# Optimization experiments

Hardware: AMD Instinct MI355X
Metric: run time of the kernel (lower is better)

Reference implementation:

```python
import jax, jax.numpy as jnp
import numpy as np

D_MODEL = 1024
N_HEADS = 16
D_K = D_MODEL // N_HEADS
B, S = 2, 2048


def setup_inputs() -> dict:
    key = jax.random.key(0)
    ks = jax.random.split(key, 9)
    scale = 1.0 / np.sqrt(D_MODEL)
    x = jax.random.normal(ks[0], (B, S, D_MODEL), dtype=jnp.float32)
    # causal mask, broadcastable to [B, H, S, S]; mask==0 -> masked
    mask = jnp.tril(jnp.ones((S, S), dtype=bool))[None, None]
    wq = jax.random.normal(ks[1], (D_MODEL, D_MODEL), dtype=jnp.float32) * scale
    bq = jnp.zeros((D_MODEL,), dtype=jnp.float32)
    wk = jax.random.normal(ks[2], (D_MODEL, D_K), dtype=jnp.float32) * scale
    bk = jnp.zeros((D_K,), dtype=jnp.float32)
    wv = jax.random.normal(ks[3], (D_MODEL, D_K), dtype=jnp.float32) * scale
    bv = jnp.zeros((D_K,), dtype=jnp.float32)
    wo = jax.random.normal(ks[4], (D_MODEL, D_MODEL), dtype=jnp.float32) * scale
    bo = jnp.zeros((D_MODEL,), dtype=jnp.float32)
    return {"x": x, "mask": mask, "wq": wq, "bq": bq, "wk": wk, "bk": bk,
            "wv": wv, "bv": bv, "wo": wo, "bo": bo}


def reference(x, mask, wq, bq, wk, bk, wv, bv, wo, bo):
    b, s, d = x.shape
    h, dk = N_HEADS, D_K
    q = (x @ wq + bq).reshape(b, s, h, dk)            # [b,s,h,dk]
    k = x @ wk + bk                                    # [b,s,dk] shared across heads (MQA)
    v = x @ wv + bv                                    # [b,s,dk]
    scores = jnp.einsum('bshd,btd->bhst', q, k) / jnp.sqrt(jnp.float32(dk))
    scores = jnp.where(mask, scores, jnp.float32(-1e9))
    attn = jax.nn.softmax(scores, axis=-1)             # [b,h,s,t]
    out = jnp.einsum('bhst,btd->bshd', attn, v).reshape(b, s, d)
    return out @ wo + bo
```

## Files before the change

### kernel.cpp

```cpp
#include <hip/hip_runtime.h>
#include <hip/hip_bf16.h>
#include <stdint.h>


typedef __attribute__((ext_vector_type(8))) short short8;
typedef __attribute__((ext_vector_type(4))) short short4_t;
typedef __attribute__((ext_vector_type(4))) float f32x4;

#define MFMA16(a, b, c) __builtin_amdgcn_mfma_f32_16x16x32_bf16((a), (b), (c), 0, 0, 0)

#define SCALE_Q 0.1803368801111244f

__device__ inline void gload_lds16(const void* g, void* l) {
  __builtin_amdgcn_global_load_lds(
      (const __attribute__((address_space(1))) void*)g,
      (__attribute__((address_space(3))) void*)l, 16, 0, 0);
}

__device__ inline float fast_exp2(float x) {
  float r;
  asm("v_exp_f32 %0, %1" : "=v"(r) : "v"(x));
  return r;
}

__device__ inline short f2bf(float f) {
  union { float f; uint32_t u; } v;
  v.f = f;
  uint32_t u = v.u;
  return (short)((u + 0x7fffu + ((u >> 16) & 1u)) >> 16);
}

__device__ inline uint32_t pk_bf16(float lo, float hi) {
  uint32_t r;
  asm("v_cvt_pk_bf16_f32 %0, %1, %2" : "=v"(r) : "v"(lo), "v"(hi));
  return r;
}

__device__ inline int imin(int a, int b) { return a < b ? a : b; }

__global__ __launch_bounds__(256) void k_prep(
    const float* __restrict__ x, const float* __restrict__ wq,
    const float* __restrict__ wk, const float* __restrict__ wv,
    const float* __restrict__ bq, const float* __restrict__ bk,
    const float* __restrict__ bv, const float* __restrict__ wo,
    short* __restrict__ xb, short* __restrict__ wqkvt,
    float* __restrict__ biasq, short* __restrict__ wot) {
  const int blk = blockIdx.x;
  const int t = threadIdx.x;
  if (blk >= 545) {
    const int base = (blk - 545) * 8192;
#pragma unroll
    for (int it = 0; it < 4; ++it) {
      const int i = base + it * 2048 + t * 8;
      const float* xp = x + i;
      short8 o;
#pragma unroll
      for (int j = 0; j < 8; ++j) o[j] = f2bf(xp[j]);
      *(short8*)(xb + i) = o;
    }
    return;
  }
  if (blk == 544) {
    for (int idx = t; idx < 1152; idx += 256)
      biasq[idx] = idx < 1024 ? bq[idx] * SCALE_Q
                              : (idx < 1088 ? bk[idx - 1024] : bv[idx - 1088]);
    return;
  }
  __shared__ float lds[64][65];
  const int j = blk;
  const float* src;
  short* dst;
  int ncol, k0, n0, row0;
  float sc = 1.f;
  if (j < 256)      { src = wq; dst = wqkvt; ncol = 1024; k0 = (j >> 4) * 64;
                      n0 = (j & 15) * 64; row0 = n0; sc = SCALE_Q; }
  else if (j < 272) { src = wk; dst = wqkvt; ncol = 64; k0 = (j - 256) * 64;
                      n0 = 0; row0 = 1024; }
  else if (j < 288) { src = wv; dst = wqkvt; ncol = 64; k0 = (j - 272) * 64;
                      n0 = 0; row0 = 1088; }
  else              { int jj = j - 288; src = wo; dst = wot; ncol = 1024;
                      k0 = (jj >> 4) * 64; n0 = (jj & 15) * 64; row0 = n0; }
#pragma unroll
  for (int i = 0; i < 4; ++i) {
    int f = i * 256 + t;
    int k = f >> 4, c = f & 15;
    const float* sp = src + (size_t)(k0 + k) * ncol + n0 + c * 4;
#pragma unroll
    for (int q = 0; q < 4; ++q) lds[k][c * 4 + q] = sp[q];
  }
  __syncthreads();
#pragma unroll
  for (int i = 0; i < 2; ++i) {
    int f = i * 256 + t;
    int n = f >> 3, kc = f & 7;
    short8 o;
#pragma unroll
    for (int q = 0; q < 8; ++q) o[q] = f2bf(lds[kc * 8 + q][n] * sc);
    *(short8*)(dst + (size_t)(row0 + n) * 1024 + k0 + kc * 8) = o;
  }
}

__global__ __launch_bounds__(256, 3) void k_gemm(const short* __restrict__ A,
                                                 const short* __restrict__ Bt,
                                                 const float* __restrict__ bias,
                                                 void* __restrict__ C, int ldc,
                                                 int out_bf16,
                                                 short* __restrict__ vt_out) {
  __shared__ short As[2][4096];
  __shared__ short Bs[2][8192];
  const int t = threadIdx.x;
  const int w = t >> 6, l = t & 63;
  const int l15 = l & 15, lhi = l >> 4;
  const int m0 = blockIdx.x * 64, n0 = blockIdx.y * 128;

  f32x4 acc[4][2];
#pragma unroll
  for (int i = 0; i < 4; ++i)
#pragma unroll
    for (int j = 0; j < 2; ++j)
#pragma unroll
      for (int r = 0; r < 4; ++r) acc[i][j][r] = 0.f;

  const int fA0 = w * 64 + l;
  const int rA0 = fA0 >> 3, gA0 = (fA0 & 7) ^ (rA0 & 7);
  const int fA1 = fA0 + 256;
  const int rA1 = fA1 >> 3, gA1 = (fA1 & 7) ^ (rA1 & 7);

  const int aoff = l15 * 128 + ((lhi ^ (l15 & 7)) << 4);
  const int coff = l15 * 128 + (((4 + lhi) ^ (l15 & 7)) << 4);

#define GEMM_STAGE(buf, k0)                                                    \
  {                                                                            \
    gload_lds16(A + (size_t)(m0 + rA0) * 1024 + (k0) + gA0 * 8,               \
                &As[buf][w * 512]);                                            \
    gload_lds16(A + (size_t)(m0 + rA1) * 1024 + (k0) + gA1 * 8,               \
                &As[buf][2048 + w * 512]);                                     \
    _Pragma("unroll")                                                          \
    for (int q = 0; q < 4; ++q) {                                              \
      int f = q * 256 + fA0;                                                   \
      int r = f >> 3, gc = (f & 7) ^ (r & 7);                                  \
      gload_lds16(Bt + (size_t)(n0 + r) * 1024 + (k0) + gc * 8,               \
                  &Bs[buf][q * 2048 + w * 512]);                               \
    }                                                                          \
  }

  GEMM_STAGE(0, 0);

  for (int ks = 0; ks < 16; ++ks) {
    const int nb = (ks + 1) & 1;
    GEMM_STAGE(nb, imin(ks + 1, 15) * 64);
    asm volatile("s_waitcnt vmcnt(6)" ::: "memory");

    const char* as = (const char*)&As[ks & 1][0];
    const char* bs = (const char*)&Bs[ks & 1][0];
    short8 afA[4], afB[4], bfA[2], bfB[2];
#pragma unroll
    for (int i = 0; i < 4; ++i) {
      afA[i] = *(const short8*)(as + i * 2048 + aoff);
      afB[i] = *(const short8*)(as + i * 2048 + coff);
    }
#pragma unroll
    for (int j = 0; j < 2; ++j) {
      bfA[j] = *(const short8*)(bs + (w * 32 + j * 16) * 128 + aoff);
      bfB[j] = *(const short8*)(bs + (w * 32 + j * 16) * 128 + coff);
    }
#pragma unroll
    for (int i = 0; i < 4; ++i)
#pragma unroll
      for (int j = 0; j < 2; ++j) {
        acc[i][j] = MFMA16(afA[i], bfA[j], acc[i][j]);
        acc[i][j] = MFMA16(afB[i], bfB[j], acc[i][j]);
      }
    __builtin_amdgcn_s_barrier();
  }
  asm volatile("s_waitcnt vmcnt(0)" ::: "memory");

#pragma unroll
  for (int j = 0; j < 2; ++j) {
    int col = n0 + w * 32 + j * 16 + l15;
    float bia = bias[col];
#pragma unroll
    for (int i = 0; i < 4; ++i) {
      int row0 = m0 + i * 16 + lhi * 4;
      if (out_bf16) {
#pragma unroll
        for (int r = 0; r < 4; ++r)
          ((short*)C)[(size_t)(row0 + r) * ldc + col] =
              (short)(pk_bf16(acc[i][j][r] + bia, 0.f) & 0xffff);
        if (vt_out != nullptr && col >= 1088) {
          const int d = col - 1088;
          const int bb = row0 >> 11, rho = row0 & 2047;
          const int T = rho >> 6, y = rho & 63;
          const int pb = 16 * ((y >> 3) & 1) + 8 * ((y >> 2) & 1) +
                         4 * ((y >> 5) & 1) + 2 * ((y >> 4) & 1);
          short* vp = vt_out + (size_t)(bb * 64 + d) * 2048 + T * 64 + pb;
          *(uint32_t*)(vp) = pk_bf16(acc[i][j][0] + bia, acc[i][j][1] + bia);
          *(uint32_t*)(vp + 32) = pk_bf16(acc[i][j][2] + bia, acc[i][j][3] + bia);
        }
      } else {
#pragma unroll
        for (int r = 0; r < 4; ++r)
          ((float*)C)[(size_t)(row0 + r) * ldc + col] = acc[i][j][r] + bia;
      }
    }
  }
#undef GEMM_STAGE
}

__global__ __launch_bounds__(512, 4) void k_attn(const short* __restrict__ qkv,
                                                 const short* __restrict__ vt,
                                                 short* __restrict__ attnb) {
  __shared__ char smem[65536];
  const int t = threadIdx.x;
  const int w = t >> 6, l = t & 63;
  const int l15 = l & 15, lhi = l >> 4;
  const int qw = w & 3, g2 = w >> 2;
  const int bx = blockIdx.x;
  const int o = bx >> 5, gg = o & 7;
  const int p = (o < 8) ? gg : 15 - gg;
  const int bh = bx & 31, b = bh >> 4, h = bh & 15;
  const int nph = p + 1;
  const short* kb = qkv + (size_t)(b * 2048) * 1152 + 1024;
  const short* vb = vt + (size_t)b * 64 * 2048;

  const int srow = w * 8 + (l >> 3);
  const int gcol = (l & 7) ^ (l >> 3);
  const short* kS = kb + (size_t)srow * 1152 + gcol * 8;
  const short* vS = vb + (size_t)srow * 2048 + gcol * 8;

  const int aoff = l15 * 128 + ((lhi ^ (l15 & 7)) << 4);
  const int coff = l15 * 128 + (((4 + lhi) ^ (l15 & 7)) << 4);

  short8 ones;
#pragma unroll
  for (int j = 0; j < 8; ++j) ones[j] = (short)0x3F80;

  const int qbase = p * 128 + qw * 32;
  const int myq0 = qbase + l15;
  const int myq1 = qbase + 16 + l15;
  const int ttdiag = qbase >> 6;

  const short* qp0 = qkv + (size_t)(b * 2048 + myq0) * 1152 + h * 64 + 8 * lhi;
  const short* qp1 = qkv + (size_t)(b * 2048 + myq1) * 1152 + h * 64 + 8 * lhi;
  short8 qa0 = *(const short8*)(qp0);
  short8 qc0 = *(const short8*)(qp0 + 32);
  short8 qa1 = *(const short8*)(qp1);
  short8 qc1 = *(const short8*)(qp1 + 32);

  f32x4 oo[2][4], o5a, o5b;
#pragma unroll
  for (int qg = 0; qg < 2; ++qg)
#pragma unroll
    for (int fd = 0; fd < 4; ++fd)
#pragma unroll
      for (int r = 0; r < 4; ++r) oo[qg][fd][r] = 0.f;
#pragma unroll
  for (int r = 0; r < 4; ++r) { o5a[r] = 0.f; o5b[r] = 0.f; }

  gload_lds16(kS, smem + w * 1024);
  gload_lds16(kS + 73728, smem + 16384 + w * 1024);
  gload_lds16(vS, smem + 32768 + w * 1024);
  gload_lds16(vS + 64, smem + 32768 + 16384 + w * 1024);
  __syncthreads();

#pragma unroll 1
  for (int i = 0; i < nph; ++i) {
    if (i + 1 < nph) {
      const int nb = (i + 1) & 1;
      const size_t ko2 = (size_t)(2 * i + 2) * 73728;
      const int vo2 = (2 * i + 2) * 64;
      gload_lds16(kS + ko2, smem + nb * 8192 + w * 1024);
      gload_lds16(kS + ko2 + 73728, smem + 16384 + nb * 8192 + w * 1024);
      gload_lds16(vS + vo2, smem + 32768 + nb * 8192 + w * 1024);
      gload_lds16(vS + vo2 + 64, smem + 32768 + 16384 + nb * 8192 + w * 1024);
      __builtin_amdgcn_sched_barrier(0);
    }

    const int tt = 2 * i + g2;
    const int cb = i & 1;

    const char* kr = smem + g2 * 16384 + cb * 8192;
    f32x4 s0[4], s1[4];
    __builtin_amdgcn_s_setprio(1);
#pragma unroll
    for (int f = 0; f < 4; ++f) {
      short8 ka = *(const short8*)(kr + f * 2048 + aoff);
      short8 kc = *(const short8*)(kr + f * 2048 + coff);
      f32x4 z0 = {0.f, 0.f, 0.f, 0.f};
      z0 = MFMA16(ka, qa0, z0);
      z0 = MFMA16(kc, qc0, z0);
      s0[f] = z0;
      f32x4 z1 = {0.f, 0.f, 0.f, 0.f};
      z1 = MFMA16(ka, qa1, z1);
      z1 = MFMA16(kc, qc1, z1);
      s1[f] = z1;
    }
    __builtin_amdgcn_s_setprio(0);

    if (tt >= ttdiag) {
      const int t0 = tt * 64;
#pragma unroll
      for (int f = 0; f < 4; ++f) {
        int kvb = t0 + f * 16 + lhi * 4;
#pragma unroll
        for (int r = 0; r < 4; ++r) {
          s0[f][r] = (kvb + r <= myq0) ? s0[f][r] : -1e30f;
          s1[f][r] = (kvb + r <= myq1) ? s1[f][r] : -1e30f;
        }
      }
    }

#pragma unroll
    for (int f = 0; f < 4; ++f)
#pragma unroll
      for (int r = 0; r < 4; ++r) {
        s0[f][r] = fast_exp2(s0[f][r]);
        s1[f][r] = fast_exp2(s1[f][r]);
      }

    union { short8 v; uint32_t d[4]; } pA0, pB0, pA1, pB1;
#pragma unroll
    for (int f = 0; f < 4; ++f) {
      pA0.d[f] = pk_bf16(s0[f][0], s0[f][1]);
      pB0.d[f] = pk_bf16(s0[f][2], s0[f][3]);
      pA1.d[f] = pk_bf16(s1[f][0], s1[f][1]);
      pB1.d[f] = pk_bf16(s1[f][2], s1[f][3]);
    }

    const char* vr = smem + 32768 + g2 * 16384 + cb * 8192;
    __builtin_amdgcn_s_setprio(1);
#pragma unroll
    for (int fd = 0; fd < 4; ++fd) {
      short8 va = *(const short8*)(vr + fd * 2048 + aoff);
      short8 vc = *(const short8*)(vr + fd * 2048 + coff);
      oo[0][fd] = MFMA16(va, pA0.v, oo[0][fd]);
      oo[0][fd] = MFMA16(vc, pB0.v, oo[0][fd]);
      oo[1][fd] = MFMA16(va, pA1.v, oo[1][fd]);
      oo[1][fd] = MFMA16(vc, pB1.v, oo[1][fd]);
    }
    o5a = MFMA16(ones, pA0.v, o5a);
    o5a = MFMA16(ones, pB0.v, o5a);
    o5b = MFMA16(ones, pA1.v, o5b);
    o5b = MFMA16(ones, pB1.v, o5b);
    __builtin_amdgcn_s_setprio(0);

    __syncthreads();
  }

  float* scr = (float*)smem;
  float* sp = scr + ((qw << 6) + l) * 34;
  if (g2 == 1) {
#pragma unroll
    for (int qg = 0; qg < 2; ++qg)
#pragma unroll
      for (int fd = 0; fd < 4; ++fd)
#pragma unroll
        for (int r = 0; r < 4; ++r) sp[qg * 16 + fd * 4 + r] = oo[qg][fd][r];
    sp[32] = o5a[0];
    sp[33] = o5b[0];
  }
  __syncthreads();
  if (g2 == 0) {
#pragma unroll
    for (int qg = 0; qg < 2; ++qg) {
      float lsum = (qg ? o5b[0] : o5a[0]) + sp[32 + qg];
      float inv = 1.f / lsum;
      int myq = qbase + qg * 16 + l15;
      short* op = attnb + (size_t)(b * 2048 + myq) * 1024 + h * 64;
#pragma unroll
      for (int fd = 0; fd < 4; ++fd) {
        union { short4_t s4; uint32_t d[2]; } ov;
        float v0 = (oo[qg][fd][0] + sp[qg * 16 + fd * 4 + 0]) * inv;
        float v1 = (oo[qg][fd][1] + sp[qg * 16 + fd * 4 + 1]) * inv;
        float v2 = (oo[qg][fd][2] + sp[qg * 16 + fd * 4 + 2]) * inv;
        float v3 = (oo[qg][fd][3] + sp[qg * 16 + fd * 4 + 3]) * inv;
        ov.d[0] = pk_bf16(v0, v1);
        ov.d[1] = pk_bf16(v2, v3);
        *(short4_t*)(op + fd * 16 + lhi * 4) = ov.s4;
      }
    }
  }
}

extern "C" void kernel_launch(void* const* d_in, const int* in_sizes, int n_in,
                              void* d_out, int out_size, void* d_ws, size_t ws_size,
                              hipStream_t stream) {
  const float* x  = (const float*)d_in[0];
  const float* wq = (const float*)d_in[2];
  const float* bq = (const float*)d_in[3];
  const float* wk = (const float*)d_in[4];
  const float* bk = (const float*)d_in[5];
  const float* wv = (const float*)d_in[6];
  const float* bv = (const float*)d_in[7];
  const float* wo = (const float*)d_in[8];
  const float* bo = (const float*)d_in[9];

  char* ws = (char*)d_ws;
  short* xb    = (short*)(ws + 0);
  short* qkv   = (short*)(ws + 8388608);
  short* wqkvt = (short*)(ws + 17825792);
  short* wot   = (short*)(ws + 20185088);
  short* vt    = (short*)(ws + 22282240);
  short* attnb = (short*)(ws + 22806528);
  float* biasq = (float*)(ws + 31195136);

  k_prep<<<1057, 256, 0, stream>>>(x, wq, wk, wv, bq, bk, bv, wo,
                                   xb, wqkvt, biasq, wot);
  k_gemm<<<dim3(64, 9), 256, 0, stream>>>(xb, wqkvt, biasq, qkv, 1152, 1, vt);
  k_attn<<<512, 512, 0, stream>>>(qkv, vt, attnb);
  k_gemm<<<dim3(64, 8), 256, 0, stream>>>(attnb, wot, bo, d_out, 1024, 0,
                                          nullptr);
}
```

Baseline: 69.66 us.

## Split attention KV range across four wave groups with 1024-thread blocks

```diff
diff --git a/kernel.cpp b/kernel.cpp
--- a/kernel.cpp
+++ b/kernel.cpp
@@ -207,26 +207,29 @@
 #undef GEMM_STAGE
 }
 
-__global__ __launch_bounds__(512, 4) void k_attn(const short* __restrict__ qkv,
-                                                 const short* __restrict__ vt,
-                                                 short* __restrict__ attnb) {
+__global__ __launch_bounds__(1024, 4) void k_attn(const short* __restrict__ qkv,
+                                                  const short* __restrict__ vt,
+                                                  short* __restrict__ attnb) {
   __shared__ char smem[65536];
   const int t = threadIdx.x;
   const int w = t >> 6, l = t & 63;
   const int l15 = l & 15, lhi = l >> 4;
-  const int qw = w & 3, g2 = w >> 2;
+  const int qw = w >> 2, kvg = w & 3;
   const int bx = blockIdx.x;
-  const int o = bx >> 5, gg = o & 7;
-  const int p = (o < 8) ? gg : 15 - gg;
+  const int o = bx >> 5;
+  const int p = 15 - o;
   const int bh = bx & 31, b = bh >> 4, h = bh & 15;
-  const int nph = p + 1;
+  const int nph = (2 * p + 5) >> 2;
   const short* kb = qkv + (size_t)(b * 2048) * 1152 + 1024;
   const short* vb = vt + (size_t)b * 64 * 2048;
 
-  const int srow = w * 8 + (l >> 3);
-  const int gcol = (l & 7) ^ (l >> 3);
-  const short* kS = kb + (size_t)srow * 1152 + gcol * 8;
-  const short* vS = vb + (size_t)srow * 2048 + gcol * 8;
+  const int f0 = t, f1 = t + 1024;
+  const int kR0 = (f0 >> 3) & 63, kJ0 = f0 >> 9, kG0 = (f0 & 7) ^ (kR0 & 7);
+  const int kR1 = (f1 >> 3) & 63, kJ1 = f1 >> 9, kG1 = (f1 & 7) ^ (kR1 & 7);
+  const short* kS0 = kb + (size_t)(kJ0 * 64 + kR0) * 1152 + kG0 * 8;
+  const short* kS1 = kb + (size_t)(kJ1 * 64 + kR1) * 1152 + kG1 * 8;
+  const short* vS0 = vb + (size_t)kR0 * 2048 + kJ0 * 64 + kG0 * 8;
+  const short* vS1 = vb + (size_t)kR1 * 2048 + kJ1 * 64 + kG1 * 8;
 
   const int aoff = l15 * 128 + ((lhi ^ (l15 & 7)) << 4);
   const int coff = l15 * 128 + (((4 + lhi) ^ (l15 & 7)) << 4);
@@ -257,29 +260,20 @@
 #pragma unroll
   for (int r = 0; r < 4; ++r) { o5a[r] = 0.f; o5b[r] = 0.f; }
 
-  gload_lds16(kS, smem + w * 1024);
-  gload_lds16(kS + 73728, smem + 16384 + w * 1024);
-  gload_lds16(vS, smem + 32768 + w * 1024);
-  gload_lds16(vS + 64, smem + 32768 + 16384 + w * 1024);
-  __syncthreads();
-
 #pragma unroll 1
   for (int i = 0; i < nph; ++i) {
-    if (i + 1 < nph) {
-      const int nb = (i + 1) & 1;
-      const size_t ko2 = (size_t)(2 * i + 2) * 73728;
-      const int vo2 = (2 * i + 2) * 64;
-      gload_lds16(kS + ko2, smem + nb * 8192 + w * 1024);
-      gload_lds16(kS + ko2 + 73728, smem + 16384 + nb * 8192 + w * 1024);
-      gload_lds16(vS + vo2, smem + 32768 + nb * 8192 + w * 1024);
-      gload_lds16(vS + vo2 + 64, smem + 32768 + 16384 + nb * 8192 + w * 1024);
-      __builtin_amdgcn_sched_barrier(0);
-    }
-
-    const int tt = 2 * i + g2;
-    const int cb = i & 1;
-
-    const char* kr = smem + g2 * 16384 + cb * 8192;
+    const size_t ko = (size_t)(4 * i) * 73728;
+    const int vo = 4 * i * 64;
+    gload_lds16(kS0 + ko, smem + f0 * 16);
+    gload_lds16(kS1 + ko, smem + f1 * 16);
+    gload_lds16(vS0 + vo, smem + 32768 + f0 * 16);
+    gload_lds16(vS1 + vo, smem + 32768 + f1 * 16);
+    asm volatile("s_waitcnt vmcnt(0)" ::: "memory");
+    __builtin_amdgcn_s_barrier();
+
+    const int tt = 4 * i + kvg;
+
+    const char* kr = (const char*)smem + kvg * 8192;
     f32x4 s0[4], s1[4];
     __builtin_amdgcn_s_setprio(1);
 #pragma unroll
@@ -298,10 +292,10 @@
     __builtin_amdgcn_s_setprio(0);
 
     if (tt >= ttdiag) {
-      const int t0 = tt * 64;
+      const int t0m = tt * 64;
 #pragma unroll
       for (int f = 0; f < 4; ++f) {
-        int kvb = t0 + f * 16 + lhi * 4;
+        int kvb = t0m + f * 16 + lhi * 4;
 #pragma unroll
         for (int r = 0; r < 4; ++r) {
           s0[f][r] = (kvb + r <= myq0) ? s0[f][r] : -1e30f;
@@ -327,7 +321,7 @@
       pB1.d[f] = pk_bf16(s1[f][2], s1[f][3]);
     }
 
-    const char* vr = smem + 32768 + g2 * 16384 + cb * 8192;
+    const char* vr = (const char*)smem + 32768 + kvg * 8192;
     __builtin_amdgcn_s_setprio(1);
 #pragma unroll
     for (int fd = 0; fd < 4; ++fd) {
@@ -344,42 +338,64 @@
     o5b = MFMA16(ones, pB1.v, o5b);
     __builtin_amdgcn_s_setprio(0);
 
-    __syncthreads();
+    __builtin_amdgcn_s_barrier();
   }
 
   float* scr = (float*)smem;
-  float* sp = scr + ((qw << 6) + l) * 34;
-  if (g2 == 1) {
-#pragma unroll
-    for (int qg = 0; qg < 2; ++qg)
-#pragma unroll
-      for (int fd = 0; fd < 4; ++fd)
-#pragma unroll
-        for (int r = 0; r < 4; ++r) sp[qg * 16 + fd * 4 + r] = oo[qg][fd][r];
-    sp[32] = o5a[0];
-    sp[33] = o5b[0];
-  }
-  __syncthreads();
-  if (g2 == 0) {
+  float* sp = scr + (size_t)(qw * 64 + l) * 34;
+
+#define MERGE_WRITE                                                            \
+  {                                                                            \
+    _Pragma("unroll")                                                          \
+    for (int qg = 0; qg < 2; ++qg)                                             \
+      _Pragma("unroll")                                                        \
+      for (int fd = 0; fd < 4; ++fd)                                           \
+        _Pragma("unroll")                                                      \
+        for (int r = 0; r < 4; ++r) sp[qg * 16 + fd * 4 + r] = oo[qg][fd][r];  \
+    sp[32] = o5a[0];                                                           \
+    sp[33] = o5b[0];                                                           \
+  }
+#define MERGE_ADD                                                              \
+  {                                                                            \
+    _Pragma("unroll")                                                          \
+    for (int qg = 0; qg < 2; ++qg)                                             \
+      _Pragma("unroll")                                                        \
+      for (int fd = 0; fd < 4; ++fd)                                           \
+        _Pragma("unroll")                                                      \
+        for (int r = 0; r < 4; ++r) oo[qg][fd][r] += sp[qg * 16 + fd * 4 + r]; \
+    o5a[0] += sp[32];                                                          \
+    o5b[0] += sp[33];                                                          \
+  }
+
+  if (kvg == 1) MERGE_WRITE;
+  __syncthreads();
+  if (kvg == 0) MERGE_ADD;
+  __syncthreads();
+  if (kvg == 3) MERGE_WRITE;
+  __syncthreads();
+  if (kvg == 2) MERGE_ADD;
+  __syncthreads();
+  if (kvg == 2) MERGE_WRITE;
+  __syncthreads();
+  if (kvg == 0) {
+    MERGE_ADD;
 #pragma unroll
     for (int qg = 0; qg < 2; ++qg) {
-      float lsum = (qg ? o5b[0] : o5a[0]) + sp[32 + qg];
+      float lsum = qg ? o5b[0] : o5a[0];
       float inv = 1.f / lsum;
       int myq = qbase + qg * 16 + l15;
       short* op = attnb + (size_t)(b * 2048 + myq) * 1024 + h * 64;
 #pragma unroll
       for (int fd = 0; fd < 4; ++fd) {
         union { short4_t s4; uint32_t d[2]; } ov;
-        float v0 = (oo[qg][fd][0] + sp[qg * 16 + fd * 4 + 0]) * inv;
-        float v1 = (oo[qg][fd][1] + sp[qg * 16 + fd * 4 + 1]) * inv;
-        float v2 = (oo[qg][fd][2] + sp[qg * 16 + fd * 4 + 2]) * inv;
-        float v3 = (oo[qg][fd][3] + sp[qg * 16 + fd * 4 + 3]) * inv;
-        ov.d[0] = pk_bf16(v0, v1);
-        ov.d[1] = pk_bf16(v2, v3);
+        ov.d[0] = pk_bf16(oo[qg][fd][0] * inv, oo[qg][fd][1] * inv);
+        ov.d[1] = pk_bf16(oo[qg][fd][2] * inv, oo[qg][fd][3] * inv);
         *(short4_t*)(op + fd * 16 + lhi * 4) = ov.s4;
       }
     }
   }
+#undef MERGE_WRITE
+#undef MERGE_ADD
 }
 
 extern "C" void kernel_launch(void* const* d_in, const int* in_sizes, int n_in,
@@ -407,7 +423,7 @@
   k_prep<<<1057, 256, 0, stream>>>(x, wq, wk, wv, bq, bk, bv, wo,
                                    xb, wqkvt, biasq, wot);
   k_gemm<<<dim3(64, 9), 256, 0, stream>>>(xb, wqkvt, biasq, qkv, 1152, 1, vt);
-  k_attn<<<512, 512, 0, stream>>>(qkv, vt, attnb);
+  k_attn<<<512, 1024, 0, stream>>>(qkv, vt, attnb);
   k_gemm<<<dim3(64, 8), 256, 0, stream>>>(attnb, wot, bo, d_out, 1024, 0,
                                           nullptr);
 }
```

Result: slower. 77.80 us (+11.7%).
